# Optimization experiments

Hardware: AMD Instinct MI355X
Metric: run time of the kernel (lower is better)

Reference implementation:

```python
import jax, jax.numpy as jnp
import numpy as np

OUT, IN = 4096, 4096
GROUP_SIZE = 128
NUMEL = OUT * IN                 # 16,777,216 int4 values
N_GROUPS = NUMEL // GROUP_SIZE   # 131,072
N_PACKED = NUMEL // 2            # 8,388,608 bytes (stored as int32 0..255)


def _dequantize_int4(q_packed, q_scales, q_zeros):
    """Unpack two 4-bit values per byte, dequant per group, reshape to (OUT, IN)."""
    low = q_packed & 0xF                     # [N_PACKED]
    high = (q_packed >> 4) & 0xF             # [N_PACKED]
    # interleave: flat[2i] = low nibble, flat[2i+1] = high nibble
    q = jnp.stack([low, high], axis=-1).reshape(NUMEL)            # [NUMEL] int
    qg = q.astype(jnp.float32).reshape(N_GROUPS, GROUP_SIZE)      # [G, group]
    w = (qg - q_zeros[:, None]) * q_scales[:, None]
    return w.reshape(OUT, IN)


def setup_inputs() -> dict:
    key = jax.random.key(0)
    k = jax.random.split(key, 6)
    x = jax.random.normal(k[0], (4, 2048, IN), dtype=jnp.float32)
    q_packed = jax.random.randint(k[1], (N_PACKED,), 0, 256, dtype=jnp.int32)
    q_scales = jax.random.uniform(k[2], (N_GROUPS,), dtype=jnp.float32) * 0.02 + 1e-3
    q_zeros = jax.random.uniform(k[3], (N_GROUPS,), dtype=jnp.float32) * 15.0
    delta_weight = jax.random.normal(k[4], (OUT, IN), dtype=jnp.float32) * 0.01
    bias = jax.random.normal(k[5], (OUT,), dtype=jnp.float32)
    return {"x": x, "q_packed": q_packed, "q_scales": q_scales,
            "q_zeros": q_zeros, "delta_weight": delta_weight, "bias": bias}


def reference(x, q_packed, q_scales, q_zeros, delta_weight, bias):
    W = _dequantize_int4(q_packed, q_scales, q_zeros)   # [OUT, IN]
    W_eff = W + delta_weight
    # F.linear: y = x @ W_eff^T + bias
    h = jnp.einsum('bsi,oi->bso', x, W_eff) + bias
    return h
```

## Files before the change

### kernel.cpp

```cpp
#include <hip/hip_runtime.h>


#define M_DIM 8192
#define N_DIM 4096
#define K_DIM 4096
#define NUMEL (N_DIM * K_DIM)

typedef _Float16 half_t;
typedef __attribute__((ext_vector_type(4))) _Float16 half4v;
typedef __attribute__((ext_vector_type(8))) _Float16 half8v;
typedef __attribute__((ext_vector_type(4))) float float4v;
typedef __attribute__((ext_vector_type(4))) int int4v;

#define KTILES 64
#define LDT 72

static __device__ __forceinline__ void gload16(const void* g, void* l) {
    __builtin_amdgcn_global_load_lds(
        (const __attribute__((address_space(1))) void*)g,
        (__attribute__((address_space(3))) void*)l, 16, 0, 0);
}

__global__ __launch_bounds__(256) void k_pack_w(
    const int* __restrict__ qp, const float* __restrict__ sc,
    const float* __restrict__ zr, const float* __restrict__ dwt,
    unsigned char* __restrict__ Wp)
{
    const long t = (long)blockIdx.x * 256 + threadIdx.x;
    const long flat = t * 8;
    const int g = (int)(flat >> 7);
    const float s = sc[g];
    const float zs = zr[g] * s;
    int4v q4 = *(const int4v*)(qp + (flat >> 1));
    float4v d0 = *(const float4v*)(dwt + flat);
    float4v d1 = *(const float4v*)(dwt + flat + 4);
    float d[8] = {d0[0], d0[1], d0[2], d0[3], d1[0], d1[1], d1[2], d1[3]};
    half8v vh;
#pragma unroll
    for (int j = 0; j < 4; ++j) {
        vh[2*j]   = (half_t)fmaf((float)(q4[j] & 15),        s, d[2*j]   - zs);
        vh[2*j+1] = (half_t)fmaf((float)((q4[j] >> 4) & 15), s, d[2*j+1] - zs);
    }
    const int n = (int)(flat >> 12);
    const int k = (int)(flat & 4095);
    const int row = n & 127;
    const int a = (row << 7) + ((k & 63) << 1);
    const int b = a ^ ((row & 7) << 4);
    *(half8v*)(Wp + (((size_t)((n >> 7) * KTILES + (k >> 6))) << 14) + b) = vh;
}

__global__ __launch_bounds__(256) void k_pack_x(
    const float* __restrict__ X, unsigned char* __restrict__ Xp)
{
    const long flat = ((long)blockIdx.x * 256 + threadIdx.x) * 8;
    float4v x0 = *(const float4v*)(X + flat);
    float4v x1 = *(const float4v*)(X + flat + 4);
    half8v vh;
    vh[0] = (half_t)x0[0]; vh[1] = (half_t)x0[1];
    vh[2] = (half_t)x0[2]; vh[3] = (half_t)x0[3];
    vh[4] = (half_t)x1[0]; vh[5] = (half_t)x1[1];
    vh[6] = (half_t)x1[2]; vh[7] = (half_t)x1[3];
    const int m = (int)(flat >> 12);
    const int k = (int)(flat & 4095);
    const int row = m & 127;
    const int a = (row << 7) + ((k & 63) << 1);
    const int b = a ^ ((row & 7) << 4);
    *(half8v*)(Xp + (((size_t)((m >> 7) * KTILES + (k >> 6))) << 14) + b) = vh;
}

#define BARX() do { __builtin_amdgcn_sched_barrier(0); \
                    __builtin_amdgcn_s_barrier(); \
                    __builtin_amdgcn_sched_barrier(0); } while(0)
#define WAITV(N) do { asm volatile("s_waitcnt vmcnt(" #N ")" ::: "memory"); \
                      __builtin_amdgcn_sched_barrier(0); } while(0)

#define READ_A(BUF, F0) do { \
_Pragma("unroll") for (int i_ = 0; i_ < 4; ++i_) { \
    const int row_ = ((F0) + i_) * 16 + fr; \
_Pragma("unroll") for (int ks_ = 0; ks_ < 2; ++ks_) { \
        const int off_ = ks_ * 64 + kg16; \
        ah[i_][ks_] = *(const half8v*)(&lds[BUF][wm][row_ * 128 + (off_ ^ swz)]); \
    } } } while(0)

#define READ_B(BUF, DST, J0) do { \
_Pragma("unroll") for (int j_ = 0; j_ < 2; ++j_) { \
    const int row_ = bbase + ((J0) + j_) * 16 + fr; \
_Pragma("unroll") for (int ks_ = 0; ks_ < 2; ++ks_) { \
        const int off_ = ks_ * 64 + kg16; \
        DST[j_][ks_] = *(const half8v*)(&lds[BUF][bhalf][row_ * 128 + (off_ ^ swz)]); \
    } } } while(0)

#define MFMA_Q(F0, N0, BREG) do { \
    __builtin_amdgcn_s_setprio(1); \
_Pragma("unroll") for (int i_ = 0; i_ < 4; ++i_) \
_Pragma("unroll") for (int j_ = 0; j_ < 2; ++j_) \
_Pragma("unroll") for (int ks_ = 0; ks_ < 2; ++ks_) \
        acc[(F0)+i_][(N0)+j_] = __builtin_amdgcn_mfma_f32_16x16x32_f16( \
            ah[i_][ks_], BREG[j_][ks_], acc[(F0)+i_][(N0)+j_], 0, 0, 0); \
    __builtin_amdgcn_s_setprio(0); \
} while(0)

__global__ __launch_bounds__(512, 2) void k_gemm8ph(
    const unsigned char* __restrict__ Apk, const unsigned char* __restrict__ Bpk,
    const float* __restrict__ bias, float* __restrict__ Y)
{
    __shared__ __align__(16) unsigned char lds[2][4][16384];

    const int tid  = threadIdx.x;
    const int lane = tid & 63;
    const int wave = tid >> 6;
    const int wm = wave >> 2;
    const int wn = wave & 3;
    const int bhalf = 2 + (wn >> 1);
    const int bbase = (wn & 1) * 64;
    const int fr   = lane & 15;
    const int kg16 = (lane >> 4) << 4;
    const int swz  = (fr & 7) << 4;

    const int wg = blockIdx.x;
    const int swg = (wg & 7) * 64 + (wg >> 3);
    const int bn = swg & 15;
    const int bm = swg >> 4;

    auto asrc = [&](int h, int tk) {
        return Apk + ((((size_t)(2 * bm + h)) * KTILES + tk) << 14);
    };
    auto bsrc = [&](int h, int tk) {
        return Bpk + ((((size_t)(2 * bn + h)) * KTILES + tk) << 14);
    };
    auto stageh = [&](int b, int h, const unsigned char* s) {
        unsigned char* d = &lds[b][h][tid << 4];
        gload16(s + (tid << 4), d);
        gload16(s + 8192 + (tid << 4), d + 8192);
    };

    half8v ah[4][2], b01[2][2], b23[2][2];
    float4v acc[8][4];
    const float4v zero4 = {0.f, 0.f, 0.f, 0.f};
#pragma unroll
    for (int i = 0; i < 8; ++i)
#pragma unroll
        for (int j = 0; j < 4; ++j) acc[i][j] = zero4;

    stageh(0, 0, asrc(0, 0)); stageh(0, 1, asrc(1, 0));
    stageh(0, 2, bsrc(0, 0)); stageh(0, 3, bsrc(1, 0));
    stageh(1, 2, bsrc(0, 1)); stageh(1, 3, bsrc(1, 1));
    WAITV(4);
    BARX();

    for (int it = 0; it < 31; ++it) {
        const int t1 = 2 * it + 1, t2 = 2 * it + 2, t3 = 2 * it + 3;
        READ_A(0, 0); READ_B(0, b01, 0);
        stageh(1, 0, asrc(0, t1)); stageh(1, 1, asrc(1, t1));
        BARX();
        MFMA_Q(0, 0, b01);
        READ_B(0, b23, 2);
        BARX();
        MFMA_Q(0, 2, b23);
        READ_A(0, 4);
        BARX();
        MFMA_Q(4, 2, b23);
        stageh(0, 2, bsrc(0, t2)); stageh(0, 3, bsrc(1, t2));
        WAITV(4);
        BARX();
        MFMA_Q(4, 0, b01);
        READ_A(1, 0); READ_B(1, b01, 0);
        stageh(0, 0, asrc(0, t2)); stageh(0, 1, asrc(1, t2));
        BARX();
        MFMA_Q(0, 0, b01);
        READ_B(1, b23, 2);
        BARX();
        MFMA_Q(0, 2, b23);
        READ_A(1, 4);
        BARX();
        MFMA_Q(4, 2, b23);
        stageh(1, 2, bsrc(0, t3)); stageh(1, 3, bsrc(1, t3));
        WAITV(4);
        BARX();
        MFMA_Q(4, 0, b01);
    }

    READ_A(0, 0); READ_B(0, b01, 0);
    stageh(1, 0, asrc(0, 63)); stageh(1, 1, asrc(1, 63));
    BARX(); MFMA_Q(0, 0, b01);
    READ_B(0, b23, 2);
    BARX(); MFMA_Q(0, 2, b23);
    READ_A(0, 4);
    BARX(); MFMA_Q(4, 2, b23);
    WAITV(0);
    BARX(); MFMA_Q(4, 0, b01);
    READ_A(1, 0); READ_B(1, b01, 0);
    BARX(); MFMA_Q(0, 0, b01);
    READ_B(1, b23, 2);
    BARX(); MFMA_Q(0, 2, b23);
    READ_A(1, 4);
    BARX(); MFMA_Q(4, 2, b23);
    MFMA_Q(4, 0, b01);

    const long m0 = (long)bm * 256 + wm * 128;
    const long n0 = (long)bn * 256 + wn * 64;
#pragma unroll
    for (int mf = 0; mf < 8; ++mf) {
        const long row = m0 + mf * 16 + (lane >> 4) * 4;
#pragma unroll
        for (int nf = 0; nf < 4; ++nf) {
            const long col = n0 + nf * 16 + (lane & 15);
            const float b = bias[col];
#pragma unroll
            for (int r = 0; r < 4; ++r)
                Y[(row + r) * N_DIM + col] = acc[mf][nf][r] + b;
        }
    }
}

__global__ __launch_bounds__(256, 2) void k_gemm_fused(
    const float* __restrict__ X, const int* __restrict__ qp,
    const float* __restrict__ sc, const float* __restrict__ zr,
    const float* __restrict__ dwt,
    const float* __restrict__ bias, float* __restrict__ Y)
{
    __shared__ __align__(16) half_t Ah[128 * LDT];
    __shared__ __align__(16) half_t Bh[128 * LDT];

    const int tid  = threadIdx.x;
    const int lane = tid & 63;
    const int wave = tid >> 6;
    const int wm = wave >> 1, wn = wave & 1;
    const int bn = blockIdx.x & 31;
    const int bm = blockIdx.x >> 5;
    const long m0 = (long)bm * 128;
    const long n0 = (long)bn * 128;
    const int fr = lane & 15;
    const int ko = (lane >> 4) * 8;

    const float4v zero4 = {0.f, 0.f, 0.f, 0.f};
    float4v acc[4][4];
#pragma unroll
    for (int i = 0; i < 4; ++i)
#pragma unroll
        for (int j = 0; j < 4; ++j) acc[i][j] = zero4;

    for (int k0 = 0; k0 < K_DIM; k0 += 64) {
        {
            const int ar = tid >> 4;
            const int ac = (tid & 15) * 4;
#pragma unroll
            for (int rr = 0; rr < 8; ++rr) {
                const int row = ar + rr * 16;
                float4v xv = *(const float4v*)(X + (m0 + row) * K_DIM + k0 + ac);
                half4v h;
#pragma unroll
                for (int j = 0; j < 4; ++j) h[j] = (half_t)xv[j];
                *(half4v*)(Ah + row * LDT + ac) = h;
            }
        }
        {
            const int cr = tid >> 3;
            const int cc = (tid & 7) * 8;
#pragma unroll
            for (int rr = 0; rr < 4; ++rr) {
                const int row = cr + rr * 32;
                const long n = n0 + row;
                const int g = (int)(n * 32 + (k0 >> 7));
                const float s = sc[g];
                const float zs = zr[g] * s;
                const long flat = n * K_DIM + k0 + cc;
                int4v q4 = *(const int4v*)(qp + (flat >> 1));
                float4v d0 = *(const float4v*)(dwt + flat);
                float4v d1 = *(const float4v*)(dwt + flat + 4);
                float d[8] = {d0[0], d0[1], d0[2], d0[3], d1[0], d1[1], d1[2], d1[3]};
                half8v vh;
#pragma unroll
                for (int j = 0; j < 4; ++j) {
                    vh[2*j]   = (half_t)fmaf((float)(q4[j] & 15),        s, d[2*j]   - zs);
                    vh[2*j+1] = (half_t)fmaf((float)((q4[j] >> 4) & 15), s, d[2*j+1] - zs);
                }
                *(half8v*)(Bh + row * LDT + cc) = vh;
            }
        }
        __syncthreads();
#pragma unroll
        for (int ks = 0; ks < 2; ++ks) {
            const int kk = ks * 32 + ko;
            half8v a2[4], b2[4];
#pragma unroll
            for (int i = 0; i < 4; ++i) {
                a2[i] = *(const half8v*)(Ah + (wm * 64 + i * 16 + fr) * LDT + kk);
                b2[i] = *(const half8v*)(Bh + (wn * 64 + i * 16 + fr) * LDT + kk);
            }
#pragma unroll
            for (int i = 0; i < 4; ++i)
#pragma unroll
                for (int j = 0; j < 4; ++j)
                    acc[i][j] = __builtin_amdgcn_mfma_f32_16x16x32_f16(
                        a2[i], b2[j], acc[i][j], 0, 0, 0);
        }
        __syncthreads();
    }

#pragma unroll
    for (int i = 0; i < 4; ++i) {
        const long mrow = m0 + wm * 64 + i * 16 + (lane >> 4) * 4;
#pragma unroll
        for (int j = 0; j < 4; ++j) {
            const long col = n0 + wn * 64 + j * 16 + (lane & 15);
            const float b = bias[col];
#pragma unroll
            for (int r = 0; r < 4; ++r)
                Y[(mrow + r) * N_DIM + col] = acc[i][j][r] + b;
        }
    }
}

extern "C" void kernel_launch(void* const* d_in, const int* in_sizes, int n_in,
                              void* d_out, int out_size, void* d_ws, size_t ws_size,
                              hipStream_t stream)
{
    const float* X  = (const float*)d_in[0];
    const int*   qp = (const int*)d_in[1];
    const float* sc = (const float*)d_in[2];
    const float* zr = (const float*)d_in[3];
    const float* dwt = (const float*)d_in[4];
    const float* bs = (const float*)d_in[5];
    float* Y = (float*)d_out;

    const size_t needB = (size_t)N_DIM * K_DIM * 2;
    const size_t needA = (size_t)M_DIM * K_DIM * 2;

    if (ws_size >= needA + needB) {
        unsigned char* Bpk = (unsigned char*)d_ws;
        unsigned char* Apk = Bpk + needB;
        k_pack_w<<<dim3(NUMEL / 8 / 256), dim3(256), 0, stream>>>(qp, sc, zr, dwt, Bpk);
        k_pack_x<<<dim3((M_DIM * (size_t)K_DIM) / 8 / 256), dim3(256), 0, stream>>>(X, Apk);
        k_gemm8ph<<<dim3((M_DIM / 256) * (N_DIM / 256)), dim3(512), 0, stream>>>(Apk, Bpk, bs, Y);
    } else {
        k_gemm_fused<<<dim3((M_DIM / 128) * (N_DIM / 128)), dim3(256), 0, stream>>>(
            X, qp, sc, zr, dwt, bs, Y);
    }
}
```

Measured before the change: 278.5 us.

## Pre-pack operands in MFMA fragment order and drop intra-tile barriers

The pack kernels now write A and B tiles in the exact per-lane fragment order the MFMA reads use. Each LDS read becomes a contiguous lane*16 offset, replacing the XOR-swizzled row addressing, and the pack kernels iterate over output order so their stores are fully contiguous. Two of the four barriers per half-iteration are removed, on the reasoning that those phases only read LDS already synchronized. Output stores use nontemporal hints. The risk is a race if the removed barriers were protecting buffer reuse, and strided global reads in the pack kernels.

```diff
diff --git a/kernel.cpp b/kernel.cpp
--- a/kernel.cpp
+++ b/kernel.cpp
@@ -26,9 +26,14 @@
     const float* __restrict__ zr, const float* __restrict__ dwt,
     unsigned char* __restrict__ Wp)
 {
-    const long t = (long)blockIdx.x * 256 + threadIdx.x;
-    const long flat = t * 8;
-    const int g = (int)(flat >> 7);
+    const size_t o = ((size_t)blockIdx.x * 256 + threadIdx.x) << 4;
+    const int chunk16 = (int)(o >> 14);
+    const int c  = (int)(o >> 10) & 15;
+    const int ln = (int)(o >> 4) & 63;
+    const int n = (chunk16 >> 6) * 128 + (c >> 1) * 16 + (ln & 15);
+    const int k = (chunk16 & 63) * 64 + (c & 1) * 32 + (ln >> 4) * 8;
+    const long flat = (long)n * K_DIM + k;
+    const int g = n * 32 + (k >> 7);
     const float s = sc[g];
     const float zs = zr[g] * s;
     int4v q4 = *(const int4v*)(qp + (flat >> 1));
@@ -41,31 +46,27 @@
         vh[2*j]   = (half_t)fmaf((float)(q4[j] & 15),        s, d[2*j]   - zs);
         vh[2*j+1] = (half_t)fmaf((float)((q4[j] >> 4) & 15), s, d[2*j+1] - zs);
     }
-    const int n = (int)(flat >> 12);
-    const int k = (int)(flat & 4095);
-    const int row = n & 127;
-    const int a = (row << 7) + ((k & 63) << 1);
-    const int b = a ^ ((row & 7) << 4);
-    *(half8v*)(Wp + (((size_t)((n >> 7) * KTILES + (k >> 6))) << 14) + b) = vh;
+    *(half8v*)(Wp + o) = vh;
 }
 
 __global__ __launch_bounds__(256) void k_pack_x(
     const float* __restrict__ X, unsigned char* __restrict__ Xp)
 {
-    const long flat = ((long)blockIdx.x * 256 + threadIdx.x) * 8;
-    float4v x0 = *(const float4v*)(X + flat);
-    float4v x1 = *(const float4v*)(X + flat + 4);
+    const size_t o = ((size_t)blockIdx.x * 256 + threadIdx.x) << 4;
+    const int chunk16 = (int)(o >> 14);
+    const int c  = (int)(o >> 10) & 15;
+    const int ln = (int)(o >> 4) & 63;
+    const int m = (chunk16 >> 6) * 128 + (c >> 1) * 16 + (ln & 15);
+    const int k = (chunk16 & 63) * 64 + (c & 1) * 32 + (ln >> 4) * 8;
+    const float* src = X + (size_t)m * K_DIM + k;
+    float4v x0 = *(const float4v*)(src);
+    float4v x1 = *(const float4v*)(src + 4);
     half8v vh;
     vh[0] = (half_t)x0[0]; vh[1] = (half_t)x0[1];
     vh[2] = (half_t)x0[2]; vh[3] = (half_t)x0[3];
     vh[4] = (half_t)x1[0]; vh[5] = (half_t)x1[1];
     vh[6] = (half_t)x1[2]; vh[7] = (half_t)x1[3];
-    const int m = (int)(flat >> 12);
-    const int k = (int)(flat & 4095);
-    const int row = m & 127;
-    const int a = (row << 7) + ((k & 63) << 1);
-    const int b = a ^ ((row & 7) << 4);
-    *(half8v*)(Xp + (((size_t)((m >> 7) * KTILES + (k >> 6))) << 14) + b) = vh;
+    *(half8v*)(Xp + o) = vh;
 }
 
 #define BARX() do { __builtin_amdgcn_sched_barrier(0); \
@@ -75,20 +76,18 @@
                       __builtin_amdgcn_sched_barrier(0); } while(0)
 
 #define READ_A(BUF, F0) do { \
-_Pragma("unroll") for (int i_ = 0; i_ < 4; ++i_) { \
-    const int row_ = ((F0) + i_) * 16 + fr; \
-_Pragma("unroll") for (int ks_ = 0; ks_ < 2; ++ks_) { \
-        const int off_ = ks_ * 64 + kg16; \
-        ah[i_][ks_] = *(const half8v*)(&lds[BUF][wm][row_ * 128 + (off_ ^ swz)]); \
-    } } } while(0)
+_Pragma("unroll") for (int i_ = 0; i_ < 4; ++i_) \
+_Pragma("unroll") for (int ks_ = 0; ks_ < 2; ++ks_) \
+        ah[i_][ks_] = *(const half8v*)(&lds[BUF][wm] \
+            [((((F0) + i_) * 2 + ks_) << 10) + lane16]); \
+    } while(0)
 
 #define READ_B(BUF, DST, J0) do { \
-_Pragma("unroll") for (int j_ = 0; j_ < 2; ++j_) { \
-    const int row_ = bbase + ((J0) + j_) * 16 + fr; \
-_Pragma("unroll") for (int ks_ = 0; ks_ < 2; ++ks_) { \
-        const int off_ = ks_ * 64 + kg16; \
-        DST[j_][ks_] = *(const half8v*)(&lds[BUF][bhalf][row_ * 128 + (off_ ^ swz)]); \
-    } } } while(0)
+_Pragma("unroll") for (int j_ = 0; j_ < 2; ++j_) \
+_Pragma("unroll") for (int ks_ = 0; ks_ < 2; ++ks_) \
+        DST[j_][ks_] = *(const half8v*)(&lds[BUF][bhalf] \
+            [bq8192 + ((((J0) + j_) * 2 + ks_) << 10) + lane16]); \
+    } while(0)
 
 #define MFMA_Q(F0, N0, BREG) do { \
     __builtin_amdgcn_s_setprio(1); \
@@ -112,10 +111,8 @@
     const int wm = wave >> 2;
     const int wn = wave & 3;
     const int bhalf = 2 + (wn >> 1);
-    const int bbase = (wn & 1) * 64;
-    const int fr   = lane & 15;
-    const int kg16 = (lane >> 4) << 4;
-    const int swz  = (fr & 7) << 4;
+    const int bq8192 = (wn & 1) << 13;
+    const int lane16 = lane << 4;
 
     const int wg = blockIdx.x;
     const int swg = (wg & 7) * 64 + (wg >> 3);
@@ -152,10 +149,8 @@
         const int t1 = 2 * it + 1, t2 = 2 * it + 2, t3 = 2 * it + 3;
         READ_A(0, 0); READ_B(0, b01, 0);
         stageh(1, 0, asrc(0, t1)); stageh(1, 1, asrc(1, t1));
-        BARX();
         MFMA_Q(0, 0, b01);
         READ_B(0, b23, 2);
-        BARX();
         MFMA_Q(0, 2, b23);
         READ_A(0, 4);
         BARX();
@@ -166,10 +161,8 @@
         MFMA_Q(4, 0, b01);
         READ_A(1, 0); READ_B(1, b01, 0);
         stageh(0, 0, asrc(0, t2)); stageh(0, 1, asrc(1, t2));
-        BARX();
         MFMA_Q(0, 0, b01);
         READ_B(1, b23, 2);
-        BARX();
         MFMA_Q(0, 2, b23);
         READ_A(1, 4);
         BARX();
@@ -208,7 +201,8 @@
             const float b = bias[col];
 #pragma unroll
             for (int r = 0; r < 4; ++r)
-                Y[(row + r) * N_DIM + col] = acc[mf][nf][r] + b;
+                __builtin_nontemporal_store(acc[mf][nf][r] + b,
+                                            &Y[(row + r) * N_DIM + col]);
         }
     }
 }
@@ -330,8 +324,8 @@
     if (ws_size >= needA + needB) {
         unsigned char* Bpk = (unsigned char*)d_ws;
         unsigned char* Apk = Bpk + needB;
-        k_pack_w<<<dim3(NUMEL / 8 / 256), dim3(256), 0, stream>>>(qp, sc, zr, dwt, Bpk);
-        k_pack_x<<<dim3((M_DIM * (size_t)K_DIM) / 8 / 256), dim3(256), 0, stream>>>(X, Apk);
+        k_pack_w<<<dim3((unsigned)(needB >> 12)), dim3(256), 0, stream>>>(qp, sc, zr, dwt, Bpk);
+        k_pack_x<<<dim3((unsigned)(needA >> 12)), dim3(256), 0, stream>>>(X, Apk);
         k_gemm8ph<<<dim3((M_DIM / 256) * (N_DIM / 256)), dim3(512), 0, stream>>>(Apk, Bpk, bs, Y);
     } else {
         k_gemm_fused<<<dim3((M_DIM / 128) * (N_DIM / 128)), dim3(256), 0, stream>>>(
```

After: 284.4 us. 1.02x slower.
